# Performance work log

Hardware: AMD Instinct MI355X
Metric: run time of the kernel (lower is better)

Reference implementation:

```python
import jax, jax.numpy as jnp
import numpy as np

# module hyperparams (match init_kwargs)
C, K, S, RATIO, GC = 64, 7, 2, 2, 16
G = C // GC                      # 4 groups
KK = K * K                       # 49
NS = int(RATIO * S)              # 4
NN = NS * NS                     # 16
PAD = (K - 1) // 2               # 3
C1_IN = G * (2 * K * GC + KK)    # 1092
C1_OUT = G * NN * KK // 10       # 313
C2_OUT = G * NN * KK             # 3136
EPS = 1e-5


def _unfold(x, k, s, p):
    # torch.nn.Unfold: patches ordered (C, ki, kj) channel-major
    B, Cc, H, W = x.shape
    xp = jnp.pad(x, ((0, 0), (0, 0), (p, p), (p, p)))
    Ho = (H + 2 * p - k) // s + 1
    Wo = (W + 2 * p - k) // s + 1
    rows = jnp.arange(Ho)[:, None] * s + jnp.arange(k)[None, :]      # (Ho,k)
    cols = jnp.arange(Wo)[:, None] * s + jnp.arange(k)[None, :]      # (Wo,k)
    pat = xp[:, :, rows[:, :, None, None], cols[None, None, :, :]]   # (B,C,Ho,k,Wo,k)
    return pat.transpose(0, 1, 3, 5, 2, 4)                            # (B,C,k,k,Ho,Wo)


def setup_inputs() -> dict:
    key = jax.random.key(0)
    ks = jax.random.split(key, 5)
    x = jax.random.normal(ks[0], (8, C, 64, 64), dtype=jnp.float32)
    w1 = jax.random.normal(ks[1], (C1_OUT, C1_IN), dtype=jnp.float32) * 0.02
    gamma = jnp.ones((C1_OUT,), dtype=jnp.float32)   # BN weight (constant_init 1)
    beta = jnp.zeros((C1_OUT,), dtype=jnp.float32)   # BN bias
    w2 = jax.random.normal(ks[2], (C2_OUT, C1_OUT), dtype=jnp.float32) * 0.02
    b2 = jnp.zeros((C2_OUT,), dtype=jnp.float32)
    return {"x": x, "w1": w1, "gamma": gamma, "beta": beta, "w2": w2, "b2": b2}


def reference(x, w1, gamma, beta, w2, b2):
    B, _, H, W = x.shape
    pat = _unfold(x, K, S, PAD)                          # (B,C,K,K,Ho,Wo)
    Ho, Wo = pat.shape[-2], pat.shape[-1]
    xg = pat.reshape(B, G, GC, K, K, Ho, Wo)
    # three axis-wise max pools -> per-pixel descriptor
    x1 = xg.max(axis=2).reshape(B, G * K * K, Ho, Wo)
    x2 = xg.max(axis=3).reshape(B, G * GC * K, Ho, Wo)
    x3 = xg.max(axis=4).reshape(B, G * GC * K, Ho, Wo)
    feat = jnp.concatenate([x1, x2, x3], axis=1)         # (B, C1_IN, Ho, Wo)
    # conv1: 1x1 conv (no bias) + BN (batch stats) + ReLU
    h = jnp.einsum('bchw,oc->bohw', feat, w1)
    mu = h.mean(axis=(0, 2, 3), keepdims=True)
    var = h.var(axis=(0, 2, 3), keepdims=True)
    h = gamma[None, :, None, None] * (h - mu) * jax.lax.rsqrt(var + EPS) + beta[None, :, None, None]
    h = jax.nn.relu(h)
    # conv2: 1x1 conv with bias
    h2 = jnp.einsum('bchw,oc->bohw', h, w2) + b2[None, :, None, None]
    wt = h2.reshape(B, G, KK, NN, Ho, Wo)
    wt = jax.nn.softmax(wt, axis=2)                      # softmax over kernel positions
    # softmax-weighted patch reduction (mean over k*k)
    xk = xg.reshape(B, G, GC, KK, Ho, Wo)
    out = jnp.einsum('bgckhw,bgknhw->bgcnhw', xk, wt) / KK
    out = out.reshape(B, C, NS, NS, Ho, Wo)
    out = out.transpose(0, 1, 4, 2, 5, 3).reshape(B, C, Ho * NS, Wo * NS)
    return out
```

## Files before the change

### kernel.cpp

```cpp
#include <hip/hip_runtime.h>

namespace {
constexpr int kB    = 8;
constexpr int kC    = 64;
constexpr int kH    = 64, kW = 64;
constexpr int kNP   = 8192;
constexpr int kC1In = 1092;
constexpr int kKP   = 1152;
constexpr int kC1Out= 313;
constexpr int kC2Out= 3136;
constexpr int kC1P  = 320;
constexpr int kRowS = 56;
constexpr int kPosS = 16 * kRowS + 8;
}

typedef __attribute__((ext_vector_type(8))) short bf16x8;
typedef __attribute__((ext_vector_type(8))) _Float16 f16x8;
typedef __attribute__((ext_vector_type(2))) _Float16 h16x2;
typedef __attribute__((ext_vector_type(4))) float f32x4;

__device__ __forceinline__ unsigned short f2bf(float f) {
    unsigned u = __float_as_uint(f);
    unsigned r = (u + 0x7fffu + ((u >> 16) & 1u)) >> 16;
    return (unsigned short)r;
}

__global__ void k_w2split(const float* __restrict__ w2, bf16x8* __restrict__ w2t) {
    int idx = blockIdx.x * 256 + threadIdx.x;
    int lane = idx & 63;
    int t = (idx >> 6) % 10;
    int k = (idx / 640) % 49;
    int g = idx / 31360;
    int n = lane & 15, c0 = t * 32 + ((lane >> 4) << 3);
    int row = g * 784 + k * 16 + n;
    bf16x8 hi;
    #pragma unroll
    for (int e = 0; e < 8; ++e) {
        int c = c0 + e;
        float v = (c < kC1Out) ? w2[(size_t)row * kC1Out + c] : 0.f;
        hi[e] = (short)f2bf(v);
    }
    w2t[idx] = hi;
}

__global__ void k_w1cvt(const float* __restrict__ w1, unsigned short* __restrict__ w1s) {
    int idx = blockIdx.x * 256 + threadIdx.x;
    if (idx >= kC1P * kKP) return;
    int r = idx / kKP, c = idx - r * kKP;
    float v = (r < kC1Out && c < kC1In) ? w1[(size_t)r * kC1In + c] : 0.f;
    w1s[idx] = f2bf(v);
}

__global__ __launch_bounds__(256) void k_feat(const float* __restrict__ x,
                                              unsigned short* __restrict__ feat_bf) {
    __shared__ float xs[16 * 7 * 40];
    int tid = threadIdx.x;
    int g = blockIdx.x, pt = blockIdx.y;
    int p0 = pt * 16;
    int b = p0 >> 10, i = (p0 >> 5) & 31, j0 = p0 & 31;
    int y0 = 2 * i - 3, xbase = 2 * j0 - 3;
    const float* xb = x + ((size_t)(b * 64 + g * 16) << 12);

    for (int idx = tid; idx < 16 * 7 * 40; idx += 256) {
        int ch = idx / 280, r2 = idx - ch * 280;
        int row = r2 / 40, col = r2 - row * 40;
        int yy = y0 + row, xx = xbase + col;
        float v = 0.f;
        if ((unsigned)yy < 64u && (unsigned)xx < 64u)
            v = xb[(ch << 12) + (yy << 6) + xx];
        xs[idx] = v;
    }
    __syncthreads();

    for (int o = tid; o < 16 * 273; o += 256) {
        int pos = o / 273, c = o - pos * 273;
        float m = -INFINITY;
        int cg;
        if (c < 49) {
            int a = c / 7, bk = c - a * 7;
            int base = a * 40 + 2 * pos + bk;
            #pragma unroll
            for (int ch = 0; ch < 16; ++ch) m = fmaxf(m, xs[ch * 280 + base]);
            cg = g * 49 + c;
        } else if (c < 161) {
            int r = c - 49;
            int ch = r / 7, bk = r - ch * 7;
            int base = ch * 280 + 2 * pos + bk;
            #pragma unroll
            for (int a = 0; a < 7; ++a) m = fmaxf(m, xs[base + a * 40]);
            cg = 196 + g * 112 + r;
        } else {
            int r = c - 161;
            int ch = r / 7, a = r - ch * 7;
            int base = ch * 280 + a * 40 + 2 * pos;
            #pragma unroll
            for (int bk = 0; bk < 7; ++bk) m = fmaxf(m, xs[base + bk]);
            cg = 644 + g * 112 + r;
        }
        feat_bf[(size_t)(p0 + pos) * kKP + cg] = f2bf(m);
    }
    if (g == 3) {
        for (int idx = tid; idx < 16 * 60; idx += 256) {
            int pos = idx / 60, c = idx - pos * 60;
            feat_bf[(size_t)(p0 + pos) * kKP + 1092 + c] = 0;
        }
    }
}

__global__ __launch_bounds__(256) void k_gemm1(
        const unsigned short* __restrict__ feat_bf, const unsigned short* __restrict__ w1s,
        float* __restrict__ h, float* __restrict__ sum_, float* __restrict__ sumsq_) {
    __shared__ unsigned short Ald[64 * 64];
    __shared__ unsigned short Bld[64 * 64];
    __shared__ float lsum[64], lsq[64];
    int tid = threadIdx.x;
    int lane = tid & 63, wv = tid >> 6;
    int row0 = blockIdx.x * 64, col0 = blockIdx.y * 64;
    int wr = wv >> 1, wc = wv & 1;
    int srow = lane >> 3;
    int soct = (lane & 7) ^ srow;
    int frow = lane & 15, fk = lane >> 4;

    f32x4 acc[2][2] = {};
    for (int k0 = 0; k0 < kKP; k0 += 64) {
        #pragma unroll
        for (int qq = 0; qq < 4; ++qq) {
            int q = wv + qq * 4;
            const unsigned short* srcbase;
            unsigned short* dst;
            int grow;
            if (q < 8) { grow = row0 + q * 8 + srow; srcbase = feat_bf; dst = Ald + q * 512; }
            else       { grow = col0 + (q - 8) * 8 + srow; srcbase = w1s; dst = Bld + (q - 8) * 512; }
            const unsigned short* src = srcbase + (size_t)grow * kKP + k0 + soct * 8;
            __builtin_amdgcn_global_load_lds(
                (const __attribute__((address_space(1))) unsigned int*)src,
                (__attribute__((address_space(3))) unsigned int*)dst, 16, 0, 0);
        }
        __syncthreads();
        #pragma unroll
        for (int ks = 0; ks < 2; ++ks) {
            int oct = ks * 4 + fk;
            bf16x8 a0, a1, b0, b1;
            { int r = wr * 32 + frow;      a0 = *(const bf16x8*)(Ald + (r * 8 + (oct ^ (r & 7))) * 8); }
            { int r = wr * 32 + 16 + frow; a1 = *(const bf16x8*)(Ald + (r * 8 + (oct ^ (r & 7))) * 8); }
            { int r = wc * 32 + frow;      b0 = *(const bf16x8*)(Bld + (r * 8 + (oct ^ (r & 7))) * 8); }
            { int r = wc * 32 + 16 + frow; b1 = *(const bf16x8*)(Bld + (r * 8 + (oct ^ (r & 7))) * 8); }
            acc[0][0] = __builtin_amdgcn_mfma_f32_16x16x32_bf16(a0, b0, acc[0][0], 0, 0, 0);
            acc[0][1] = __builtin_amdgcn_mfma_f32_16x16x32_bf16(a0, b1, acc[0][1], 0, 0, 0);
            acc[1][0] = __builtin_amdgcn_mfma_f32_16x16x32_bf16(a1, b0, acc[1][0], 0, 0, 0);
            acc[1][1] = __builtin_amdgcn_mfma_f32_16x16x32_bf16(a1, b1, acc[1][1], 0, 0, 0);
        }
        __syncthreads();
    }

    if (tid < 64) { lsum[tid] = 0.f; lsq[tid] = 0.f; }
    __syncthreads();
    #pragma unroll
    for (int i = 0; i < 2; ++i) {
        int mrow = row0 + wr * 32 + i * 16 + (lane >> 4) * 4;
        #pragma unroll
        for (int j = 0; j < 2; ++j) {
            int col_l = wc * 32 + j * 16 + (lane & 15);
            float s = 0.f, sq = 0.f;
            #pragma unroll
            for (int r = 0; r < 4; ++r) {
                float v = acc[i][j][r];
                h[(size_t)(mrow + r) * kC1P + col0 + col_l] = v;
                s += v; sq += v * v;
            }
            atomicAdd(&lsum[col_l], s);
            atomicAdd(&lsq[col_l], sq);
        }
    }
    __syncthreads();
    if (tid < 64 && col0 + tid < kC1Out) {
        atomicAdd(&sum_[col0 + tid], lsum[tid]);
        atomicAdd(&sumsq_[col0 + tid], lsq[tid]);
    }
}

__global__ void k_finalize(const float* __restrict__ sum_, const float* __restrict__ sumsq_,
                           const float* __restrict__ gamma, const float* __restrict__ beta,
                           float* __restrict__ scale, float* __restrict__ shift) {
    int o = blockIdx.x * 256 + threadIdx.x;
    if (o >= kC1Out) return;
    float mu  = sum_[o]   * (1.f / kNP);
    float var = sumsq_[o] * (1.f / kNP) - mu * mu;
    float sc  = gamma[o] * rsqrtf(var + 1e-5f);
    scale[o] = sc;
    shift[o] = beta[o] - mu * sc;
}

__global__ void k_split_h(const float* __restrict__ h,
                          const float* __restrict__ scale, const float* __restrict__ shift,
                          bf16x8* __restrict__ ht_hi) {
    int idx = blockIdx.x * 256 + threadIdx.x;
    int lane = idx & 63;
    int t = (idx >> 6) % 10;
    int ptile = idx / 640;
    int pos = ptile * 16 + (lane & 15);
    int c0 = t * 32 + ((lane >> 4) << 3);
    float vv[8];
    *(float4*)&vv[0] = *(const float4*)(h + (size_t)pos * kC1P + c0);
    *(float4*)&vv[4] = *(const float4*)(h + (size_t)pos * kC1P + c0 + 4);
    bf16x8 hi;
    #pragma unroll
    for (int e = 0; e < 8; ++e) {
        int c = c0 + e;
        float v = (c < kC1Out) ? fmaxf(vv[e] * scale[c] + shift[c], 0.f) : 0.f;
        hi[e] = (short)f2bf(v);
    }
    ht_hi[idx] = hi;
}

__global__ __launch_bounds__(512) void k_fused(
        const bf16x8* __restrict__ ht_hi, const bf16x8* __restrict__ w2t,
        const float* __restrict__ b2, const float* __restrict__ x,
        float* __restrict__ out) {
    __shared__ _Float16 wtb[32 * kPosS];
    __shared__ float invt[512];
    int tid = threadIdx.x;
    int lane = tid & 63, wv = tid >> 6;
    int bid = blockIdx.x;
    int g = bid >> 8, pt = bid & 255;

    bf16x8 a0[10], a1[10];
    {
        const bf16x8* hb = ht_hi + (size_t)(pt * 2) * 640 + lane;
        #pragma unroll
        for (int t = 0; t < 10; ++t) { a0[t] = hb[t * 64]; a1[t] = hb[640 + t * 64]; }
    }

    int col = lane & 15, rgrp = lane >> 4;
    for (int k = wv; k < 49; k += 8) {
        f32x4 acc0 = {0.f, 0.f, 0.f, 0.f};
        f32x4 acc1 = {0.f, 0.f, 0.f, 0.f};
        const bf16x8* wb = w2t + ((size_t)(g * 49 + k) * 10) * 64 + lane;
        #pragma unroll
        for (int t = 0; t < 10; ++t) {
            bf16x8 bh = wb[t * 64];
            acc0 = __builtin_amdgcn_mfma_f32_16x16x32_bf16(a0[t], bh, acc0, 0, 0, 0);
            acc1 = __builtin_amdgcn_mfma_f32_16x16x32_bf16(a1[t], bh, acc1, 0, 0, 0);
        }
        float bias = b2[g * 784 + k * 16 + col];
        #pragma unroll
        for (int r = 0; r < 4; ++r) {
            int pos = rgrp * 4 + r;
            wtb[pos * kPosS + col * kRowS + k]        = (_Float16)(acc0[r] + bias);
            wtb[(pos + 16) * kPosS + col * kRowS + k] = (_Float16)(acc1[r] + bias);
        }
    }
    __syncthreads();

    {
        int pos = tid >> 4, n = tid & 15;
        _Float16* base = wtb + pos * kPosS + n * kRowS;
        f16x8 row[7];
        #pragma unroll
        for (int c = 0; c < 7; ++c) row[c] = *(const f16x8*)(base + c * 8);
        float m = -INFINITY;
        #pragma unroll
        for (int c = 0; c < 7; ++c)
            #pragma unroll
            for (int e = 0; e < 8; ++e)
                if (c * 8 + e < 49) m = fmaxf(m, (float)row[c][e]);
        float s = 0.f;
        #pragma unroll
        for (int c = 0; c < 7; ++c) {
            f16x8 ee;
            #pragma unroll
            for (int e = 0; e < 8; ++e) {
                if (c * 8 + e < 49) {
                    float ex = __expf((float)row[c][e] - m);
                    s += ex;
                    ee[e] = (_Float16)ex;
                } else ee[e] = (_Float16)0.f;
            }
            *(f16x8*)(base + c * 8) = ee;
        }
        invt[tid] = 1.f / (s * 49.f);
    }
    __syncthreads();

    {
        int pos = tid & 31, c16 = tid >> 5;
        int p = pt * 32 + pos;
        int b = p >> 10, i = (p >> 5) & 31, j = p & 31;
        int y0 = 2 * i - 3, x0c = 2 * j - 3;
        const float* xc = x + (((size_t)b * 64 + g * 16 + c16) << 12);
        h16x2 patch2[28];
        #pragma unroll
        for (int a = 0; a < 7; ++a) {
            int yy = y0 + a;
            #pragma unroll
            for (int bk = 0; bk < 7; ++bk) {
                int kk = a * 7 + bk, xx = x0c + bk;
                float v = ((unsigned)yy < 64u && (unsigned)xx < 64u)
                        ? xc[(yy << 6) + xx] : 0.f;
                patch2[kk >> 1][kk & 1] = (_Float16)v;
            }
        }
        patch2[24][1] = (_Float16)0.f;
        patch2[25] = (h16x2)(_Float16)0.f;
        patch2[26] = (h16x2)(_Float16)0.f;
        patch2[27] = (h16x2)(_Float16)0.f;

        const _Float16* prow = wtb + pos * kPosS;
        float* outb = out + (((size_t)b * 64 + g * 16 + c16) << 14);
        #pragma unroll
        for (int n1 = 0; n1 < 4; ++n1) {
            f32x4 st;
            #pragma unroll
            for (int n2 = 0; n2 < 4; ++n2) {
                int n = n1 * 4 + n2;
                const f16x8* row = (const f16x8*)(prow + n * kRowS);
                float acc = 0.f;
                #pragma unroll
                for (int c = 0; c < 7; ++c) {
                    f16x8 w = row[c];
                    #pragma unroll
                    for (int q = 0; q < 4; ++q) {
                        h16x2 wp; wp[0] = w[2 * q]; wp[1] = w[2 * q + 1];
                        acc = __builtin_amdgcn_fdot2(patch2[c * 4 + q], wp, acc, false);
                    }
                }
                st[n2] = acc * invt[pos * 16 + n];
            }
            *(f32x4*)(outb + (i * 4 + n1) * 128 + j * 4) = st;
        }
    }
}

extern "C" void kernel_launch(void* const* d_in, const int* in_sizes, int n_in,
                              void* d_out, int out_size, void* d_ws, size_t ws_size,
                              hipStream_t stream) {
    const float* x     = (const float*)d_in[0];
    const float* w1    = (const float*)d_in[1];
    const float* gamma = (const float*)d_in[2];
    const float* beta  = (const float*)d_in[3];
    const float* w2    = (const float*)d_in[4];
    const float* b2    = (const float*)d_in[5];
    float* out = (float*)d_out;

    float* ws = (float*)d_ws;
    unsigned short* feat_bf = (unsigned short*)ws;
    float* h       = ws + 4718592;
    float* w2t_f   = h + 2621440;
    unsigned short* w1s = (unsigned short*)(w2t_f + 501760);
    float* sum_   = w2t_f + 501760 + 184320;
    float* sumsq_ = sum_ + 320;
    float* scale  = sumsq_ + 320;
    float* shift  = scale + 320;

    bf16x8* ht_hi = (bf16x8*)ws;
    bf16x8* w2t   = (bf16x8*)w2t_f;

    hipMemsetAsync(sum_, 0, 2 * 320 * sizeof(float), stream);
    k_w2split<<<490, 256, 0, stream>>>(w2, w2t);
    k_w1cvt<<<(kC1P * kKP + 255) / 256, 256, 0, stream>>>(w1, w1s);
    k_feat<<<dim3(4, 512), 256, 0, stream>>>(x, feat_bf);
    k_gemm1<<<dim3(kNP / 64, 5), 256, 0, stream>>>(feat_bf, w1s, h, sum_, sumsq_);
    k_finalize<<<2, 256, 0, stream>>>(sum_, sumsq_, gamma, beta, scale, shift);
    k_split_h<<<1280, 256, 0, stream>>>(h, scale, shift, ht_hi);
    k_fused<<<1024, 512, 0, stream>>>(ht_hi, w2t, b2, x, out);
}
```

Measured before the change: 129.8 us.

## Restructure fused GEMM2 loop into padded slot batches and hoist patch loads

The w2 tiles are padded from 49 to 56 kernel-position slots per group, so each wave runs a fixed 7 slots. The wave processes them in batches of 4 and 3 with independent accumulators, loading A fragments per t-step instead of holding all 20 in registers. The x patch gather for the final reduction is moved to the start of the kernel so its global loads overlap the GEMM and softmax. This raises MFMA-level parallelism and reuse of each A load, in exchange for some wasted MFMAs on padded slots and longer live ranges for the patch registers.

```diff
diff --git a/kernel.cpp b/kernel.cpp
--- a/kernel.cpp
+++ b/kernel.cpp
@@ -12,6 +12,7 @@
 constexpr int kC1P  = 320;
 constexpr int kRowS = 56;
 constexpr int kPosS = 16 * kRowS + 8;
+constexpr int kSlots= 56;
 }
 
 typedef __attribute__((ext_vector_type(8))) short bf16x8;
@@ -29,16 +30,18 @@
     int idx = blockIdx.x * 256 + threadIdx.x;
     int lane = idx & 63;
     int t = (idx >> 6) % 10;
-    int k = (idx / 640) % 49;
-    int g = idx / 31360;
+    int k = (idx / 640) % kSlots;
+    int g = idx / (kSlots * 640);
     int n = lane & 15, c0 = t * 32 + ((lane >> 4) << 3);
-    int row = g * 784 + k * 16 + n;
-    bf16x8 hi;
-    #pragma unroll
-    for (int e = 0; e < 8; ++e) {
-        int c = c0 + e;
-        float v = (c < kC1Out) ? w2[(size_t)row * kC1Out + c] : 0.f;
-        hi[e] = (short)f2bf(v);
+    bf16x8 hi = {};
+    if (k < 49) {
+        int row = g * 784 + k * 16 + n;
+        #pragma unroll
+        for (int e = 0; e < 8; ++e) {
+            int c = c0 + e;
+            float v = (c < kC1Out) ? w2[(size_t)row * kC1Out + c] : 0.f;
+            hi[e] = (short)f2bf(v);
+        }
     }
     w2t[idx] = hi;
 }
@@ -213,6 +216,39 @@
     ht_hi[idx] = hi;
 }
 
+template<int NS>
+__device__ __forceinline__ void gemm_slots(int s0,
+        const bf16x8* __restrict__ hb, const bf16x8* __restrict__ wb0,
+        const float* __restrict__ b2, _Float16* wtb,
+        int g, int wv, int col, int rgrp) {
+    f32x4 acc0[NS], acc1[NS];
+    #pragma unroll
+    for (int s = 0; s < NS; ++s) { acc0[s] = (f32x4){0,0,0,0}; acc1[s] = (f32x4){0,0,0,0}; }
+    #pragma unroll
+    for (int t = 0; t < 10; ++t) {
+        bf16x8 a0 = hb[t * 64], a1 = hb[640 + t * 64];
+        #pragma unroll
+        for (int s = 0; s < NS; ++s) {
+            bf16x8 bh = wb0[((s0 + s) * 80 + t) * 64];
+            acc0[s] = __builtin_amdgcn_mfma_f32_16x16x32_bf16(a0, bh, acc0[s], 0, 0, 0);
+            acc1[s] = __builtin_amdgcn_mfma_f32_16x16x32_bf16(a1, bh, acc1[s], 0, 0, 0);
+        }
+    }
+    #pragma unroll
+    for (int s = 0; s < NS; ++s) {
+        int k = wv + (s0 + s) * 8;
+        if (k < 49) {
+            float bias = b2[g * 784 + k * 16 + col];
+            #pragma unroll
+            for (int r = 0; r < 4; ++r) {
+                int pos = rgrp * 4 + r;
+                wtb[pos * kPosS + col * kRowS + k]        = (_Float16)(acc0[s][r] + bias);
+                wtb[(pos + 16) * kPosS + col * kRowS + k] = (_Float16)(acc1[s][r] + bias);
+            }
+        }
+    }
+}
+
 __global__ __launch_bounds__(512) void k_fused(
         const bf16x8* __restrict__ ht_hi, const bf16x8* __restrict__ w2t,
         const float* __restrict__ b2, const float* __restrict__ x,
@@ -224,32 +260,33 @@
     int bid = blockIdx.x;
     int g = bid >> 8, pt = bid & 255;
 
-    bf16x8 a0[10], a1[10];
-    {
-        const bf16x8* hb = ht_hi + (size_t)(pt * 2) * 640 + lane;
-        #pragma unroll
-        for (int t = 0; t < 10; ++t) { a0[t] = hb[t * 64]; a1[t] = hb[640 + t * 64]; }
-    }
+    int pp = tid & 31, c16p = tid >> 5;
+    int p4 = pt * 32 + pp;
+    int b4 = p4 >> 10, i4 = (p4 >> 5) & 31, j4 = p4 & 31;
+    int y04 = 2 * i4 - 3, x04 = 2 * j4 - 3;
+    const float* xc4 = x + (((size_t)b4 * 64 + g * 16 + c16p) << 12);
+    h16x2 patch2[28];
+    #pragma unroll
+    for (int a = 0; a < 7; ++a) {
+        int yy = y04 + a;
+        #pragma unroll
+        for (int bk = 0; bk < 7; ++bk) {
+            int kk = a * 7 + bk, xx = x04 + bk;
+            float v = ((unsigned)yy < 64u && (unsigned)xx < 64u)
+                    ? xc4[(yy << 6) + xx] : 0.f;
+            patch2[kk >> 1][kk & 1] = (_Float16)v;
+        }
+    }
+    patch2[24][1] = (_Float16)0.f;
+    patch2[25] = (h16x2)(_Float16)0.f;
+    patch2[26] = (h16x2)(_Float16)0.f;
+    patch2[27] = (h16x2)(_Float16)0.f;
 
     int col = lane & 15, rgrp = lane >> 4;
-    for (int k = wv; k < 49; k += 8) {
-        f32x4 acc0 = {0.f, 0.f, 0.f, 0.f};
-        f32x4 acc1 = {0.f, 0.f, 0.f, 0.f};
-        const bf16x8* wb = w2t + ((size_t)(g * 49 + k) * 10) * 64 + lane;
-        #pragma unroll
-        for (int t = 0; t < 10; ++t) {
-            bf16x8 bh = wb[t * 64];
-            acc0 = __builtin_amdgcn_mfma_f32_16x16x32_bf16(a0[t], bh, acc0, 0, 0, 0);
-            acc1 = __builtin_amdgcn_mfma_f32_16x16x32_bf16(a1[t], bh, acc1, 0, 0, 0);
-        }
-        float bias = b2[g * 784 + k * 16 + col];
-        #pragma unroll
-        for (int r = 0; r < 4; ++r) {
-            int pos = rgrp * 4 + r;
-            wtb[pos * kPosS + col * kRowS + k]        = (_Float16)(acc0[r] + bias);
-            wtb[(pos + 16) * kPosS + col * kRowS + k] = (_Float16)(acc1[r] + bias);
-        }
-    }
+    const bf16x8* hb  = ht_hi + (size_t)(pt * 2) * 640 + lane;
+    const bf16x8* wb0 = w2t + (size_t)(g * kSlots + wv) * 640 + lane;
+    gemm_slots<4>(0, hb, wb0, b2, wtb, g, wv, col, rgrp);
+    gemm_slots<3>(4, hb, wb0, b2, wtb, g, wv, col, rgrp);
     __syncthreads();
 
     {
@@ -283,30 +320,8 @@
     __syncthreads();
 
     {
-        int pos = tid & 31, c16 = tid >> 5;
-        int p = pt * 32 + pos;
-        int b = p >> 10, i = (p >> 5) & 31, j = p & 31;
-        int y0 = 2 * i - 3, x0c = 2 * j - 3;
-        const float* xc = x + (((size_t)b * 64 + g * 16 + c16) << 12);
-        h16x2 patch2[28];
-        #pragma unroll
-        for (int a = 0; a < 7; ++a) {
-            int yy = y0 + a;
-            #pragma unroll
-            for (int bk = 0; bk < 7; ++bk) {
-                int kk = a * 7 + bk, xx = x0c + bk;
-                float v = ((unsigned)yy < 64u && (unsigned)xx < 64u)
-                        ? xc[(yy << 6) + xx] : 0.f;
-                patch2[kk >> 1][kk & 1] = (_Float16)v;
-            }
-        }
-        patch2[24][1] = (_Float16)0.f;
-        patch2[25] = (h16x2)(_Float16)0.f;
-        patch2[26] = (h16x2)(_Float16)0.f;
-        patch2[27] = (h16x2)(_Float16)0.f;
-
-        const _Float16* prow = wtb + pos * kPosS;
-        float* outb = out + (((size_t)b * 64 + g * 16 + c16) << 14);
+        const _Float16* prow = wtb + pp * kPosS;
+        float* outb = out + (((size_t)b4 * 64 + g * 16 + c16p) << 14);
         #pragma unroll
         for (int n1 = 0; n1 < 4; ++n1) {
             f32x4 st;
@@ -324,9 +339,9 @@
                         acc = __builtin_amdgcn_fdot2(patch2[c * 4 + q], wp, acc, false);
                     }
                 }
-                st[n2] = acc * invt[pos * 16 + n];
+                st[n2] = acc * invt[pp * 16 + n];
             }
-            *(f32x4*)(outb + (i * 4 + n1) * 128 + j * 4) = st;
+            *(f32x4*)(outb + (i4 * 4 + n1) * 128 + j4 * 4) = st;
         }
     }
 }
@@ -346,8 +361,8 @@
     unsigned short* feat_bf = (unsigned short*)ws;
     float* h       = ws + 4718592;
     float* w2t_f   = h + 2621440;
-    unsigned short* w1s = (unsigned short*)(w2t_f + 501760);
-    float* sum_   = w2t_f + 501760 + 184320;
+    unsigned short* w1s = (unsigned short*)(w2t_f + 573440);
+    float* sum_   = w2t_f + 573440 + 184320;
     float* sumsq_ = sum_ + 320;
     float* scale  = sumsq_ + 320;
     float* shift  = scale + 320;
@@ -356,7 +371,7 @@
     bf16x8* w2t   = (bf16x8*)w2t_f;
 
     hipMemsetAsync(sum_, 0, 2 * 320 * sizeof(float), stream);
-    k_w2split<<<490, 256, 0, stream>>>(w2, w2t);
+    k_w2split<<<560, 256, 0, stream>>>(w2, w2t);
     k_w1cvt<<<(kC1P * kKP + 255) / 256, 256, 0, stream>>>(w1, w1s);
     k_feat<<<dim3(4, 512), 256, 0, stream>>>(x, feat_bf);
     k_gemm1<<<dim3(kNP / 64, 5), 256, 0, stream>>>(feat_bf, w1s, h, sum_, sumsq_);
```

Measured after the change: 144.7 us. 11.5% more time.
